# Performance work log

Measured on AMD Instinct MI355X. Metric: run time of the kernel, lower is better.

## Reference

```python
import jax, jax.numpy as jnp
import numpy as np

LEAKY_SLOPE = 0.2  # PyG GATv2Conv default negative_slope


def gatv2_layer(x, src, dst, Wl, Wr, att, bias, concat):
    """PyG GATv2Conv (eval mode, dropout off, self-loops already in src/dst).
    x: [N, Din]; Wl/Wr: [Din, H*C]; att: [H, C]; bias: [H*C] or [C].
    """
    N = x.shape[0]
    H, C = att.shape
    xl = (x @ Wl).reshape(N, H, C)   # source transform
    xr = (x @ Wr).reshape(N, H, C)   # target transform
    # per-edge GATv2 score: att . leakyrelu(x_l[j] + x_r[i])
    e = jax.nn.leaky_relu(xl[src] + xr[dst], negative_slope=LEAKY_SLOPE)  # [E, H, C]
    score = jnp.einsum('ehc,hc->eh', e, att)                              # [E, H]
    # segment softmax over incoming edges of each dst node
    m = jax.ops.segment_max(score, dst, num_segments=N)                   # [N, H]
    a = jnp.exp(score - m[dst])
    denom = jax.ops.segment_sum(a, dst, num_segments=N)                   # [N, H]
    alpha = a / denom[dst]                                                # [E, H]
    out = jax.ops.segment_sum(xl[src] * alpha[..., None], dst, num_segments=N)  # [N, H, C]
    out = out.reshape(N, H * C) if concat else out.mean(axis=1)
    return out + bias


def setup_inputs() -> dict:
    key = jax.random.key(0)
    ks = jax.random.split(key, 10)
    N, D, E = 20000, 128, 320000
    HID, HEADS, OUT = 64, 8, 32
    x = jax.random.normal(ks[0], (N, D), dtype=jnp.float32)
    edge_index = jax.random.randint(ks[1], (2, E), 0, N)
    glorot = lambda k, shape, fan: jax.random.normal(k, shape, jnp.float32) * (1.0 / np.sqrt(fan))
    W1l = glorot(ks[2], (D, HEADS * HID), D)
    W1r = glorot(ks[3], (D, HEADS * HID), D)
    att1 = glorot(ks[4], (HEADS, HID), HID)
    b1 = jnp.zeros((HEADS * HID,), jnp.float32)
    W2l = glorot(ks[5], (HEADS * HID, 64), HEADS * HID)
    W2r = glorot(ks[6], (HEADS * HID, 64), HEADS * HID)
    att2 = glorot(ks[7], (1, 64), 64)
    b2 = jnp.zeros((64,), jnp.float32)
    Wlin = glorot(ks[8], (64, OUT), 64)
    blin = jnp.zeros((OUT,), jnp.float32)
    return {"x": x, "edge_index": edge_index, "W1l": W1l, "W1r": W1r, "att1": att1,
            "b1": b1, "W2l": W2l, "W2r": W2r, "att2": att2, "b2": b2,
            "Wlin": Wlin, "blin": blin}


def reference(x, edge_index, W1l, W1r, att1, b1, W2l, W2r, att2, b2, Wlin, blin):
    N = x.shape[0]
    loop = jnp.arange(N)
    src = jnp.concatenate([edge_index[0], loop])  # PyG add_self_loops=True
    dst = jnp.concatenate([edge_index[1], loop])
    h = jax.nn.elu(gatv2_layer(x, src, dst, W1l, W1r, att1, b1, concat=True))
    h = jax.nn.elu(gatv2_layer(h, src, dst, W2l, W2r, att2, b2, concat=False))
    return jax.nn.elu(h @ Wlin + blin)
```

## Files before the change

### kernel.cpp

```cpp
#include <hip/hip_runtime.h>
#include <hip/hip_bf16.h>

typedef __attribute__((ext_vector_type(8))) short short8;
typedef __attribute__((ext_vector_type(4))) short shortx4;
typedef __attribute__((ext_vector_type(4))) float floatx4;
typedef __attribute__((ext_vector_type(2))) float float2v;
typedef __attribute__((ext_vector_type(4))) int int4v;
typedef __attribute__((ext_vector_type(2))) int int2v;

__device__ __forceinline__ float b2f(short s) {
    unsigned u = ((unsigned)(unsigned short)s) << 16;
    float f; __builtin_memcpy(&f, &u, 4); return f;
}
__device__ __forceinline__ short f2b(float f) {
    __hip_bfloat16 hb = __float2bfloat16(f);
    unsigned short us; __builtin_memcpy(&us, &hb, 2);
    return (short)us;
}
__device__ __forceinline__ float2v bpair(int p) {
    unsigned ulo = ((unsigned)p) << 16;
    unsigned uhi = ((unsigned)p) & 0xFFFF0000u;
    float flo, fhi;
    __builtin_memcpy(&flo, &ulo, 4);
    __builtin_memcpy(&fhi, &uhi, 4);
    float2v r; r.x = flo; r.y = fhi; return r;
}

__global__ void prep_all(const float* __restrict__ W1l, const float* __restrict__ W1r,
                         const float* __restrict__ W2l, const float* __restrict__ W2r,
                         short* __restrict__ w1t, short* __restrict__ w2t,
                         const int* __restrict__ esrc, const int* __restrict__ edst,
                         int E, int N, int* __restrict__ counts, int* __restrict__ srcs) {
    int tid = blockIdx.x * blockDim.x + threadIdx.x;
    int ET = E + N;
    if (tid < ET) {
        int d, s;
        if (tid < E) { d = edst[tid]; s = esrc[tid]; }
        else { d = tid - E; s = d; }
        int pos = atomicAdd(&counts[d], 1);
        if (pos < 64) srcs[(d << 6) + pos] = s;
    }
    int idx = tid;
    if (idx < 131072) {
        int n = idx >> 7, k = idx & 127;
        float v = (n < 512) ? W1l[k * 512 + n] : W1r[k * 512 + (n - 512)];
        w1t[idx] = f2b(v);
        return;
    }
    idx -= 131072;
    if (idx < 65536) {
        int n = idx >> 9, k = idx & 511;
        float v = (n < 64) ? W2l[k * 64 + n] : W2r[k * 64 + (n - 64)];
        w2t[idx] = f2b(v);
    }
}

__global__ __launch_bounds__(256) void gemm1(const float* __restrict__ X,
                                             const short* __restrict__ Bt,
                                             short* __restrict__ xl1, short* __restrict__ xr1,
                                             int M) {
    __shared__ short As[64 * 136];
    __shared__ short Bs[128 * 136];
    int t = threadIdx.x;
    int w = t >> 6, L = t & 63, q = L >> 4, s = L & 15;
    int M0 = blockIdx.y * 64, NB = blockIdx.x * 256;
    #pragma unroll
    for (int i = 0; i < 8; ++i) {
        int c = t + i * 256;
        int r = c >> 5, col = (c & 31) * 4;
        int gr = M0 + r;
        floatx4 v = {};
        if (gr < M) v = *(const floatx4*)(X + (size_t)gr * 128 + col);
        shortx4 s4;
        #pragma unroll
        for (int j = 0; j < 4; ++j) s4[j] = f2b(v[j]);
        *(shortx4*)(&As[r * 136 + col]) = s4;
    }
    short8 a[4];
    #pragma unroll
    for (int tile = 0; tile < 2; ++tile) {
        int N0 = NB + tile * 128;
        if (tile) __syncthreads();
        #pragma unroll
        for (int i = 0; i < 8; ++i) {
            int c = t + i * 256;
            int r = c >> 4, col = (c & 15) * 8;
            short8 v = *(const short8*)(Bt + (size_t)(N0 + r) * 128 + col);
            *(short8*)(&Bs[r * 136 + col]) = v;
        }
        __syncthreads();
        if (tile == 0) {
            #pragma unroll
            for (int kk = 0; kk < 4; ++kk)
                a[kk] = *(const short8*)(&As[(w * 16 + s) * 136 + kk * 32 + q * 8]);
        }
        floatx4 acc[8] = {};
        #pragma unroll
        for (int tt = 0; tt < 8; ++tt) {
            #pragma unroll
            for (int kk = 0; kk < 4; ++kk) {
                short8 b = *(const short8*)(&Bs[(tt * 16 + s) * 136 + kk * 32 + q * 8]);
                acc[tt] = __builtin_amdgcn_mfma_f32_16x16x32_bf16(a[kk], b, acc[tt], 0, 0, 0);
            }
        }
        __syncthreads();
        #pragma unroll
        for (int tt = 0; tt < 8; ++tt) {
            #pragma unroll
            for (int rg = 0; rg < 4; ++rg) {
                int rl = w * 16 + q * 4 + rg;
                Bs[rl * 136 + tt * 16 + s] = f2b(acc[tt][rg]);
            }
        }
        __syncthreads();
        short* Cb = (N0 < 512) ? xl1 : xr1;
        int cb = (N0 < 512) ? N0 : N0 - 512;
        #pragma unroll
        for (int i = 0; i < 4; ++i) {
            int c = t + i * 256;
            int r = c >> 4, col = (c & 15) * 8;
            int row = M0 + r;
            if (row < M) {
                short8 v = *(const short8*)(&Bs[r * 136 + col]);
                *(short8*)(Cb + (size_t)row * 512 + cb + col) = v;
            }
        }
    }
}

__global__ __launch_bounds__(256) void gemm2(const short* __restrict__ A,
                                             const short* __restrict__ Bt,
                                             short* __restrict__ C, int M) {
    __shared__ short As[32 * 72];
    __shared__ short Bs[64 * 72];
    int t = threadIdx.x;
    int w = t >> 6, L = t & 63, q = L >> 4, s = L & 15;
    int rw = (w >> 1) * 16, cw = (w & 1) * 32;
    int M0 = blockIdx.x * 32, N0 = blockIdx.y * 64;
    floatx4 acc[2] = {};
    for (int k0 = 0; k0 < 512; k0 += 64) {
        {
            int r = t >> 3, col = (t & 7) * 8;
            int gr = M0 + r;
            short8 v = {};
            if (gr < M) v = *(const short8*)(A + (size_t)gr * 512 + k0 + col);
            *(short8*)(&As[r * 72 + col]) = v;
        }
        #pragma unroll
        for (int i = 0; i < 2; ++i) {
            int c = t + i * 256;
            int r = c >> 3, col = (c & 7) * 8;
            short8 v = *(const short8*)(Bt + (size_t)(N0 + r) * 512 + k0 + col);
            *(short8*)(&Bs[r * 72 + col]) = v;
        }
        __syncthreads();
        #pragma unroll
        for (int kk = 0; kk < 2; ++kk) {
            short8 a = *(const short8*)(&As[(rw + s) * 72 + kk * 32 + q * 8]);
            #pragma unroll
            for (int tt = 0; tt < 2; ++tt) {
                short8 b = *(const short8*)(&Bs[(cw + tt * 16 + s) * 72 + kk * 32 + q * 8]);
                acc[tt] = __builtin_amdgcn_mfma_f32_16x16x32_bf16(a, b, acc[tt], 0, 0, 0);
            }
        }
        __syncthreads();
    }
    #pragma unroll
    for (int tt = 0; tt < 2; ++tt) {
        #pragma unroll
        for (int rg = 0; rg < 4; ++rg) {
            int rl = rw + q * 4 + rg;
            As[rl * 72 + cw + tt * 16 + s] = f2b(acc[tt][rg]);
        }
    }
    __syncthreads();
    {
        int r = t >> 3, col = (t & 7) * 8;
        int row = M0 + r;
        if (row < M) {
            short8 v = *(const short8*)(&As[r * 72 + col]);
            *(short8*)(C + (size_t)row * 128 + N0 + col) = v;
        }
    }
}

__global__ void gat_l1(const short* __restrict__ xl, const short* __restrict__ xr,
                       const int* __restrict__ counts, const int* __restrict__ srcs,
                       const float* __restrict__ att, const float* __restrict__ bias,
                       short* __restrict__ h1, int Nn) {
    int i = (blockIdx.x * blockDim.x + threadIdx.x) >> 6;
    if (i >= Nn) return;
    int L = threadIdx.x & 63;
    int c0 = L * 8;
    float2v xrv[4], at[4];
    {
        int4v x4 = *(const int4v*)(xr + (size_t)i * 512 + c0);
        #pragma unroll
        for (int c = 0; c < 4; ++c) {
            xrv[c] = bpair(x4[c]);
            at[c].x = att[c0 + 2 * c];
            at[c].y = att[c0 + 2 * c + 1];
        }
    }
    float2v acc[4] = {};
    float dnm = 0.f;
    int k = i << 6;
    int deg = counts[i]; deg = deg > 64 ? 64 : deg;
    int ke = k + deg;
    for (; k + 1 < ke; k += 2) {
        int j0 = srcs[k], j1 = srcs[k + 1];
        int4v a4 = *(const int4v*)(xl + (size_t)j0 * 512 + c0);
        int4v b4 = *(const int4v*)(xl + (size_t)j1 * 512 + c0);
        float2v v0[4], v1[4];
        float2v p0 = {}, p1 = {};
        #pragma unroll
        for (int c = 0; c < 4; ++c) {
            v0[c] = bpair(a4[c]);
            float2v tv = v0[c] + xrv[c];
            p0 += at[c] * __builtin_elementwise_max(tv, 0.2f * tv);
            v1[c] = bpair(b4[c]);
            float2v tw = v1[c] + xrv[c];
            p1 += at[c] * __builtin_elementwise_max(tw, 0.2f * tw);
        }
        float s0 = p0.x + p0.y, s1 = p1.x + p1.y;
        s0 += __shfl_xor(s0, 1, 64); s0 += __shfl_xor(s0, 2, 64); s0 += __shfl_xor(s0, 4, 64);
        s1 += __shfl_xor(s1, 1, 64); s1 += __shfl_xor(s1, 2, 64); s1 += __shfl_xor(s1, 4, 64);
        float e0 = __expf(s0), e1 = __expf(s1);
        dnm += e0 + e1;
        float2v e02; e02.x = e0; e02.y = e0;
        float2v e12; e12.x = e1; e12.y = e1;
        #pragma unroll
        for (int c = 0; c < 4; ++c) {
            acc[c] += e02 * v0[c];
            acc[c] += e12 * v1[c];
        }
    }
    if (k < ke) {
        int j = srcs[k];
        int4v a4 = *(const int4v*)(xl + (size_t)j * 512 + c0);
        float2v v0[4], p0 = {};
        #pragma unroll
        for (int c = 0; c < 4; ++c) {
            v0[c] = bpair(a4[c]);
            float2v tv = v0[c] + xrv[c];
            p0 += at[c] * __builtin_elementwise_max(tv, 0.2f * tv);
        }
        float s0 = p0.x + p0.y;
        s0 += __shfl_xor(s0, 1, 64); s0 += __shfl_xor(s0, 2, 64); s0 += __shfl_xor(s0, 4, 64);
        float e0 = __expf(s0);
        dnm += e0;
        float2v e02; e02.x = e0; e02.y = e0;
        #pragma unroll
        for (int c = 0; c < 4; ++c) acc[c] += e02 * v0[c];
    }
    float inv = 1.f / dnm;
    short8 o8;
    #pragma unroll
    for (int c = 0; c < 4; ++c) {
        float ox = fmaf(acc[c].x, inv, bias[c0 + 2 * c]);
        float oy = fmaf(acc[c].y, inv, bias[c0 + 2 * c + 1]);
        ox = ox > 0.f ? ox : __expf(ox) - 1.f;
        oy = oy > 0.f ? oy : __expf(oy) - 1.f;
        o8[2 * c] = f2b(ox);
        o8[2 * c + 1] = f2b(oy);
    }
    *(short8*)(h1 + (size_t)i * 512 + c0) = o8;
}

__global__ __launch_bounds__(256) void gat_l2_fin(const short* __restrict__ x2,
                        const int* __restrict__ counts, const int* __restrict__ srcs,
                        const float* __restrict__ att, const float* __restrict__ bias,
                        const float* __restrict__ Wlin, const float* __restrict__ blin,
                        float* __restrict__ out, int Nn) {
    __shared__ float Ws[2048];
    __shared__ float bs[32];
    __shared__ float h2s[4][64];
    int t = threadIdx.x;
    for (int idx = t; idx < 2048; idx += 256) Ws[idx] = Wlin[idx];
    if (t < 32) bs[t] = blin[t];
    __syncthreads();
    int w = t >> 6, L = t & 63;
    int i = blockIdx.x * 4 + w;
    if (i >= Nn) return;
    int g = L >> 4;
    int c4 = (L & 15) * 4;
    float2v xrv[2], at[2];
    {
        int2v xv = *(const int2v*)(x2 + (size_t)i * 128 + 64 + c4);
        xrv[0] = bpair(xv.x);
        xrv[1] = bpair(xv.y);
        floatx4 a4 = *(const floatx4*)(att + c4);
        at[0].x = a4[0]; at[0].y = a4[1];
        at[1].x = a4[2]; at[1].y = a4[3];
    }
    float dnm = 0.f;
    float2v acc0 = {}, acc1 = {};
    int kb = i << 6;
    int deg = counts[i]; deg = deg > 64 ? 64 : deg;
    int ke = kb + deg;
    for (int k0 = kb; k0 < ke; k0 += 4) {
        int k = k0 + g;
        bool val = k < ke;
        int j = srcs[val ? k : kb];
        int2v vv = *(const int2v*)(x2 + (size_t)j * 128 + c4);
        float2v v0 = bpair(vv.x), v1 = bpair(vv.y);
        float2v t0 = v0 + xrv[0], t1 = v1 + xrv[1];
        float2v pp = at[0] * __builtin_elementwise_max(t0, 0.2f * t0)
                   + at[1] * __builtin_elementwise_max(t1, 0.2f * t1);
        float p = pp.x + pp.y;
        p += __shfl_xor(p, 1, 64); p += __shfl_xor(p, 2, 64);
        p += __shfl_xor(p, 4, 64); p += __shfl_xor(p, 8, 64);
        float e = val ? __expf(p) : 0.f;
        dnm += e;
        float2v e2; e2.x = e; e2.y = e;
        acc0 += e2 * v0;
        acc1 += e2 * v1;
    }
    #pragma unroll
    for (int m = 16; m <= 32; m <<= 1) {
        dnm += __shfl_xor(dnm, m, 64);
        acc0.x += __shfl_xor(acc0.x, m, 64);
        acc0.y += __shfl_xor(acc0.y, m, 64);
        acc1.x += __shfl_xor(acc1.x, m, 64);
        acc1.y += __shfl_xor(acc1.y, m, 64);
    }
    float inv = 1.f / dnm;
    floatx4 bv = *(const floatx4*)(bias + c4);
    float o0 = fmaf(acc0.x, inv, bv[0]);
    float o1 = fmaf(acc0.y, inv, bv[1]);
    float o2 = fmaf(acc1.x, inv, bv[2]);
    float o3 = fmaf(acc1.y, inv, bv[3]);
    o0 = o0 > 0.f ? o0 : __expf(o0) - 1.f;
    o1 = o1 > 0.f ? o1 : __expf(o1) - 1.f;
    o2 = o2 > 0.f ? o2 : __expf(o2) - 1.f;
    o3 = o3 > 0.f ? o3 : __expf(o3) - 1.f;
    if (L < 16) {
        floatx4 hv; hv[0] = o0; hv[1] = o1; hv[2] = o2; hv[3] = o3;
        *(floatx4*)(&h2s[w][c4]) = hv;
    }
    int oc = L & 31;
    float accl = 0.f;
    #pragma unroll
    for (int kk = 0; kk < 16; ++kk) {
        floatx4 h = *(const floatx4*)(&h2s[w][kk * 4]);
        accl = fmaf(h[0], Ws[(kk * 4 + 0) * 32 + oc], accl);
        accl = fmaf(h[1], Ws[(kk * 4 + 1) * 32 + oc], accl);
        accl = fmaf(h[2], Ws[(kk * 4 + 2) * 32 + oc], accl);
        accl = fmaf(h[3], Ws[(kk * 4 + 3) * 32 + oc], accl);
    }
    if (L < 32) {
        float r = accl + bs[oc];
        r = r > 0.f ? r : __expf(r) - 1.f;
        out[(size_t)i * 32 + oc] = r;
    }
}

extern "C" void kernel_launch(void* const* d_in, const int* in_sizes, int n_in,
                              void* d_out, int out_size, void* d_ws, size_t ws_size,
                              hipStream_t stream) {
    const float* x    = (const float*)d_in[0];
    const int*   ei   = (const int*)d_in[1];
    const float* W1l  = (const float*)d_in[2];
    const float* W1r  = (const float*)d_in[3];
    const float* att1 = (const float*)d_in[4];
    const float* b1   = (const float*)d_in[5];
    const float* W2l  = (const float*)d_in[6];
    const float* W2r  = (const float*)d_in[7];
    const float* att2 = (const float*)d_in[8];
    const float* b2   = (const float*)d_in[9];
    const float* Wlin = (const float*)d_in[10];
    const float* blin = (const float*)d_in[11];

    const int N  = in_sizes[0] / 128;
    const int E  = in_sizes[1] / 2;
    const int ET = E + N;

    char* w = (char*)d_ws;
    size_t cur = 0;
    auto take = [&](size_t bytes) -> void* {
        void* p = w + cur;
        cur = (cur + bytes + 255) & ~(size_t)255;
        return p;
    };
    int*   counts = (int*)take((size_t)N * 4);
    int*   srcs   = (int*)take((size_t)N * 64 * 4);
    short* w1t    = (short*)take((size_t)1024 * 128 * 2);
    short* w2t    = (short*)take((size_t)128 * 512 * 2);
    short* xl1    = (short*)take((size_t)N * 512 * 2);
    short* xr1    = (short*)take((size_t)N * 512 * 2);
    short* h1     = (short*)take((size_t)N * 512 * 2);
    short* x2     = (short*)take((size_t)N * 128 * 2);

    hipMemsetAsync(counts, 0, (size_t)N * 4, stream);
    int nprep = ET > 196608 ? ET : 196608;
    prep_all<<<(nprep + 255) / 256, 256, 0, stream>>>(W1l, W1r, W2l, W2r, w1t, w2t,
                                                      ei, ei + E, E, N, counts, srcs);

    gemm1<<<dim3(4, (N + 63) / 64), 256, 0, stream>>>(x, w1t, xl1, xr1, N);
    gat_l1<<<(N + 3) / 4, 256, 0, stream>>>(xl1, xr1, counts, srcs, att1, b1, h1, N);

    gemm2<<<dim3((N + 31) / 32, 2), 256, 0, stream>>>(h1, w2t, x2, N);
    gat_l2_fin<<<(N + 3) / 4, 256, 0, stream>>>(x2, counts, srcs, att2, b2, Wlin, blin,
                                                (float*)d_out, N);
}
```

Before: 213.4 us.

## Merge CSR build, W2 transpose and layer-1 GEMM into one launch

Combines the edge-bucketing pass, the W2 bf16 transpose and the first GEMM into a single kernel, with block ranges choosing the role. The GEMM blocks now read fp32 W1l/W1r directly and transpose-convert them into shared memory instead of using a pre-transposed bf16 copy. This removes one kernel launch and the w1t round trip, and lets the atomic CSR work overlap with the GEMM. In exchange, every GEMM block redoes the W1 conversion with strided scalar shared-memory stores, which may cause bank conflicts.

After: 222.3 us. +4.2%, slower.

```diff
diff --git a/kernel.cpp b/kernel.cpp
--- a/kernel.cpp
+++ b/kernel.cpp
@@ -26,51 +26,52 @@
     float2v r; r.x = flo; r.y = fhi; return r;
 }
 
-__global__ void prep_all(const float* __restrict__ W1l, const float* __restrict__ W1r,
-                         const float* __restrict__ W2l, const float* __restrict__ W2r,
-                         short* __restrict__ w1t, short* __restrict__ w2t,
-                         const int* __restrict__ esrc, const int* __restrict__ edst,
-                         int E, int N, int* __restrict__ counts, int* __restrict__ srcs) {
-    int tid = blockIdx.x * blockDim.x + threadIdx.x;
-    int ET = E + N;
-    if (tid < ET) {
-        int d, s;
-        if (tid < E) { d = edst[tid]; s = esrc[tid]; }
-        else { d = tid - E; s = d; }
-        int pos = atomicAdd(&counts[d], 1);
-        if (pos < 64) srcs[(d << 6) + pos] = s;
-    }
-    int idx = tid;
-    if (idx < 131072) {
-        int n = idx >> 7, k = idx & 127;
-        float v = (n < 512) ? W1l[k * 512 + n] : W1r[k * 512 + (n - 512)];
-        w1t[idx] = f2b(v);
-        return;
-    }
-    idx -= 131072;
-    if (idx < 65536) {
-        int n = idx >> 9, k = idx & 511;
-        float v = (n < 64) ? W2l[k * 64 + n] : W2r[k * 64 + (n - 64)];
-        w2t[idx] = f2b(v);
-    }
-}
-
-__global__ __launch_bounds__(256) void gemm1(const float* __restrict__ X,
-                                             const short* __restrict__ Bt,
-                                             short* __restrict__ xl1, short* __restrict__ xr1,
-                                             int M) {
+__global__ __launch_bounds__(256) void csr_gemm1(
+        const int* __restrict__ esrc, const int* __restrict__ edst, int E, int N,
+        int* __restrict__ counts, int* __restrict__ srcs,
+        const float* __restrict__ X,
+        const float* __restrict__ W1l, const float* __restrict__ W1r,
+        const float* __restrict__ W2l, const float* __restrict__ W2r,
+        short* __restrict__ w2t,
+        short* __restrict__ xl1, short* __restrict__ xr1,
+        int gcsr, int ggemm) {
     __shared__ short As[64 * 136];
     __shared__ short Bs[128 * 136];
     int t = threadIdx.x;
+    int bx = blockIdx.x;
+    if (bx < gcsr) {
+        int tid = bx * 256 + t;
+        int ET = E + N;
+        if (tid < ET) {
+            int d, s;
+            if (tid < E) { d = edst[tid]; s = esrc[tid]; }
+            else { d = tid - E; s = d; }
+            int pos = atomicAdd(&counts[d], 1);
+            if (pos < 64) srcs[(d << 6) + pos] = s;
+        }
+        return;
+    }
+    if (bx >= gcsr + ggemm) {
+        int gid = (bx - gcsr - ggemm) * 256 + t;
+        #pragma unroll
+        for (int j = 0; j < 8; ++j) {
+            int idx = gid * 8 + j;
+            int n = idx >> 9, k = idx & 511;
+            float v = (n < 64) ? W2l[k * 64 + n] : W2r[k * 64 + (n - 64)];
+            w2t[idx] = f2b(v);
+        }
+        return;
+    }
+    int gi = bx - gcsr;
     int w = t >> 6, L = t & 63, q = L >> 4, s = L & 15;
-    int M0 = blockIdx.y * 64, NB = blockIdx.x * 256;
+    int M0 = (gi >> 2) * 64, NB = (gi & 3) * 256;
     #pragma unroll
     for (int i = 0; i < 8; ++i) {
         int c = t + i * 256;
         int r = c >> 5, col = (c & 31) * 4;
         int gr = M0 + r;
         floatx4 v = {};
-        if (gr < M) v = *(const floatx4*)(X + (size_t)gr * 128 + col);
+        if (gr < N) v = *(const floatx4*)(X + (size_t)gr * 128 + col);
         shortx4 s4;
         #pragma unroll
         for (int j = 0; j < 4; ++j) s4[j] = f2b(v[j]);
@@ -80,13 +81,15 @@
     #pragma unroll
     for (int tile = 0; tile < 2; ++tile) {
         int N0 = NB + tile * 128;
+        const float* Wsrc = (N0 < 512) ? W1l : W1r;
+        int nbase = (N0 < 512) ? N0 : N0 - 512;
         if (tile) __syncthreads();
-        #pragma unroll
-        for (int i = 0; i < 8; ++i) {
-            int c = t + i * 256;
-            int r = c >> 4, col = (c & 15) * 8;
-            short8 v = *(const short8*)(Bt + (size_t)(N0 + r) * 128 + col);
-            *(short8*)(&Bs[r * 136 + col]) = v;
+        for (int i = 0; i < 32; ++i) {
+            int flat = t + i * 256;
+            int k = flat >> 6, n = (flat & 63) * 2;
+            float2v v = *(const float2v*)(Wsrc + (size_t)k * 512 + nbase + n);
+            Bs[n * 136 + k] = f2b(v.x);
+            Bs[(n + 1) * 136 + k] = f2b(v.y);
         }
         __syncthreads();
         if (tile == 0) {
@@ -120,7 +123,7 @@
             int c = t + i * 256;
             int r = c >> 4, col = (c & 15) * 8;
             int row = M0 + r;
-            if (row < M) {
+            if (row < N) {
                 short8 v = *(const short8*)(&Bs[r * 136 + col]);
                 *(short8*)(Cb + (size_t)row * 512 + cb + col) = v;
             }
@@ -384,7 +387,6 @@
     };
     int*   counts = (int*)take((size_t)N * 4);
     int*   srcs   = (int*)take((size_t)N * 64 * 4);
-    short* w1t    = (short*)take((size_t)1024 * 128 * 2);
     short* w2t    = (short*)take((size_t)128 * 512 * 2);
     short* xl1    = (short*)take((size_t)N * 512 * 2);
     short* xr1    = (short*)take((size_t)N * 512 * 2);
@@ -392,11 +394,14 @@
     short* x2     = (short*)take((size_t)N * 128 * 2);
 
     hipMemsetAsync(counts, 0, (size_t)N * 4, stream);
-    int nprep = ET > 196608 ? ET : 196608;
-    prep_all<<<(nprep + 255) / 256, 256, 0, stream>>>(W1l, W1r, W2l, W2r, w1t, w2t,
-                                                      ei, ei + E, E, N, counts, srcs);
-
-    gemm1<<<dim3(4, (N + 63) / 64), 256, 0, stream>>>(x, w1t, xl1, xr1, N);
+
+    int gcsr  = (ET + 255) / 256;
+    int ggemm = 4 * ((N + 63) / 64);
+    int gw2t  = 65536 / (256 * 8);
+    csr_gemm1<<<gcsr + ggemm + gw2t, 256, 0, stream>>>(
+        ei, ei + E, E, N, counts, srcs, x, W1l, W1r, W2l, W2r, w2t,
+        xl1, xr1, gcsr, ggemm);
+
     gat_l1<<<(N + 3) / 4, 256, 0, stream>>>(xl1, xr1, counts, srcs, att1, b1, h1, N);
 
     gemm2<<<dim3((N + 31) / 32, 2), 256, 0, stream>>>(h1, w2t, x2, N);
```
